# Kernel optimization log

Hardware: AMD Instinct MI355X
Metric: run time of the kernel (lower is better)

Reference implementation:

```python
import jax, jax.numpy as jnp
import numpy as np
import math

B, T, IN_DIM = 4, 1024, 64
D, H, L, DFF = 1024, 16, 4, 4096
N_STEPS = 24
MAXLEN = 2048
DK = D // H


def _pos_encoding(max_len, d):
    pos = np.arange(max_len, dtype=np.float32)[:, None]
    div = np.exp(np.arange(0, d, 2, dtype=np.float32) * (-math.log(10000.0) / d))
    pe = np.zeros((max_len, d), dtype=np.float32)
    pe[:, 0::2] = np.sin(pos * div)
    pe[:, 1::2] = np.cos(pos * div)
    return jnp.asarray(pe)

_PE = _pos_encoding(MAXLEN, D)


def _lin(x, W, b):
    # torch Linear convention: W is (out, in)
    return x @ W.T + b


def _mha(q, kv, Wq, bq, Wk, bk, Wv, bv, Wo, bo):
    Bq, Tq, _ = q.shape
    Tk = kv.shape[1]
    Qh = _lin(q, Wq, bq).reshape(Bq, Tq, H, DK).transpose(0, 2, 1, 3)
    Kh = _lin(kv, Wk, bk).reshape(Bq, Tk, H, DK).transpose(0, 2, 1, 3)
    Vh = _lin(kv, Wv, bv).reshape(Bq, Tk, H, DK).transpose(0, 2, 1, 3)
    scores = jnp.einsum('bhqd,bhkd->bhqk', Qh, Kh) / math.sqrt(DK)
    probs = jax.nn.softmax(scores, axis=-1)
    out = jnp.einsum('bhqk,bhkd->bhqd', probs, Vh)
    out = out.transpose(0, 2, 1, 3).reshape(Bq, Tq, D)
    return _lin(out, Wo, bo)


def _ffn(x, W1, b1, W2, b2):
    return _lin(jax.nn.relu(_lin(x, W1, b1)), W2, b2)


def _ln(x, g, b, eps=1e-5):
    mu = jnp.mean(x, axis=-1, keepdims=True)
    var = jnp.var(x, axis=-1, keepdims=True)
    return (x - mu) / jnp.sqrt(var + eps) * g + b


def setup_inputs() -> dict:
    key = jax.random.key(0)
    ks = iter(jax.random.split(key, 64))
    def w(shape, s=0.02):
        return jax.random.normal(next(ks), shape, jnp.float32) * s
    inp = {'x': jax.random.normal(next(ks), (B, T, IN_DIM), jnp.float32)}
    inp['in_W'] = w((D, IN_DIM)); inp['in_b'] = jnp.zeros((D,), jnp.float32)
    for p in ['enc', 'dec']:
        for n in ['Wq', 'Wk', 'Wv', 'Wo']:
            inp[f'{p}_{n}'] = w((L, D, D))
            inp[f'{p}_b{n[1].lower()}'] = jnp.zeros((L, D), jnp.float32)
    for p in ['ffe', 'ffd']:
        inp[f'{p}_W1'] = w((DFF, D)); inp[f'{p}_b1'] = jnp.zeros((DFF,), jnp.float32)
        inp[f'{p}_W2'] = w((D, DFF)); inp[f'{p}_b2'] = jnp.zeros((D,), jnp.float32)
    for p in ['ne', 'nd']:
        inp[f'{p}_g'] = jnp.ones((D,), jnp.float32); inp[f'{p}_b'] = jnp.zeros((D,), jnp.float32)
    inp['out_W'] = w((1, D)); inp['out_b'] = jnp.zeros((1,), jnp.float32)
    inp['temb_W'] = w((D, 1)); inp['temb_b'] = jnp.zeros((D,), jnp.float32)
    return inp


def reference(x, in_W, in_b,
              enc_Wq, enc_bq, enc_Wk, enc_bk, enc_Wv, enc_bv, enc_Wo, enc_bo,
              ffe_W1, ffe_b1, ffe_W2, ffe_b2, ne_g, ne_b,
              dec_Wq, dec_bq, dec_Wk, dec_bk, dec_Wv, dec_bv, dec_Wo, dec_bo,
              ffd_W1, ffd_b1, ffd_W2, ffd_b2, nd_g, nd_b,
              out_W, out_b, temb_W, temb_b):
    batch, seq, _ = x.shape
    h = _lin(x, in_W, in_b) + _PE[:seq]
    for l in range(L):
        h = _mha(h, h, enc_Wq[l], enc_bq[l], enc_Wk[l], enc_bk[l],
                 enc_Wv[l], enc_bv[l], enc_Wo[l], enc_bo[l])
        h = _ln(h + _ffn(h, ffe_W1, ffe_b1, ffe_W2, ffe_b2), ne_g, ne_b)
    dec = jnp.zeros((batch, 1, D), x.dtype)
    preds = []
    for _ in range(N_STEPS):
        d = dec + _PE[:dec.shape[1]]
        for l in range(L):
            # same layer weights used for self- and cross-attention, as in source
            d = _mha(d, d, dec_Wq[l], dec_bq[l], dec_Wk[l], dec_bk[l],
                     dec_Wv[l], dec_bv[l], dec_Wo[l], dec_bo[l])
            d = _mha(d, h, dec_Wq[l], dec_bq[l], dec_Wk[l], dec_bk[l],
                     dec_Wv[l], dec_bv[l], dec_Wo[l], dec_bo[l])
            d = _ln(d + _ffn(d, ffd_W1, ffd_b1, ffd_W2, ffd_b2), nd_g, nd_b)
        step = _lin(d[:, -1, :], out_W, out_b)        # (B, 1)
        preds.append(step[:, None, :])                 # (B, 1, 1)
        emb = _lin(step, temb_W, temb_b)[:, None, :]   # (B, 1, D)
        dec = jnp.concatenate([dec, emb], axis=1)
    return jnp.concatenate(preds, axis=1)              # (B, n_steps, 1)
```

## Files before the change

### kernel.cpp

```cpp
#include <hip/hip_runtime.h>
#include <math.h>

#define DM    1024
#define NH    16
#define DKH   64
#define NL    4
#define DFFN  4096
#define BB    4
#define TT    1024
#define NSTEP 24
#define BT    (BB*TT)
#define MD    (BB*NSTEP)
#define CSPLIT 8
#define CKEYS  (TT/CSPLIT)
#define PSTRIDE ((size_t)MD*DM)

typedef __attribute__((ext_vector_type(8))) short s16x8;
typedef __attribute__((ext_vector_type(4))) short s16x4;
typedef __attribute__((ext_vector_type(4))) float f32x4;

__device__ inline short f2b(float f){
  unsigned u = __float_as_uint(f);
  u += 0x7fffu + ((u>>16)&1u);
  return (short)(u>>16);
}
__device__ inline float b2f(short h){
  return __uint_as_float(((unsigned)(unsigned short)h)<<16);
}

__device__ inline float wave_sum(float v){
  #pragma unroll
  for (int off=1; off<64; off<<=1) v += __shfl_xor(v, off, 64);
  return v;
}

__global__ __launch_bounds__(256)
void split_kernel(const float* __restrict__ X, short* __restrict__ Hi,
                  short* __restrict__ Lo, int n8)
{
  const size_t i = (size_t)blockIdx.x*256 + threadIdx.x;
  if (i >= (size_t)n8) return;
  const float4 v0 = *(const float4*)(X + i*8);
  const float4 v1 = *(const float4*)(X + i*8 + 4);
  const float f[8] = {v0.x,v0.y,v0.z,v0.w,v1.x,v1.y,v1.z,v1.w};
  s16x8 hv, lv;
  #pragma unroll
  for (int e=0;e<8;e++){
    const short h = f2b(f[e]);
    hv[e] = h;
    lv[e] = f2b(f[e] - b2f(h));
  }
  *(s16x8*)(Hi + i*8) = hv;
  *(s16x8*)(Lo + i*8) = lv;
}

__global__ void zero_kernel(float* __restrict__ p, int n) {
  int i = blockIdx.x*256 + threadIdx.x;
  if (i < n) p[i] = 0.f;
}

__global__ __launch_bounds__(256)
void k_transpose(const float* __restrict__ A, float* __restrict__ At)
{
  __shared__ float tile[32][33];
  const int bx = blockIdx.x & 31, by = blockIdx.x >> 5;
  const int x0 = bx*32, y0 = by*32;
  const int tid = threadIdx.x;
  for (int i=tid; i<1024; i+=256){
    const int r = i>>5, c = i&31;
    tile[r][c] = A[(size_t)(y0+r)*DM + x0+c];
  }
  __syncthreads();
  for (int i=tid; i<1024; i+=256){
    const int r = i>>5, c = i&31;
    At[(size_t)(x0+r)*DM + y0+c] = tile[c][r];
  }
}

__global__ __launch_bounds__(256)
void k_bc(const float* __restrict__ Wq, const float* __restrict__ bo,
          const float* __restrict__ bq, float* __restrict__ bc)
{
  const int row = blockIdx.x, tid = threadIdx.x;
  float s = 0.f;
  for (int j=tid; j<DM; j+=256) s += Wq[(size_t)row*DM + j]*bo[j];
  s = wave_sum(s);
  __shared__ float r4[4];
  if ((tid&63)==0) r4[tid>>6] = s;
  __syncthreads();
  if (tid==0) bc[row] = r4[0]+r4[1]+r4[2]+r4[3] + bq[row];
}

__global__ __launch_bounds__(256)
void add_pe_split(const float* __restrict__ h, short* __restrict__ Hi,
                  short* __restrict__ Lo)
{
  const int row = blockIdx.x;
  const int pos = row & (TT-1);
  const int d = threadIdx.x*4;
  const float4 a = *(const float4*)(h + (size_t)row*DM + d);
  const float c1 = -9.210340371976184f / 1024.0f;
  const float e0 = expf((float)d * c1);
  const float e1 = expf((float)(d+2) * c1);
  const float a0 = (float)pos * e0, a1 = (float)pos * e1;
  const float v[4] = {a.x + sinf(a0), a.y + cosf(a0), a.z + sinf(a1), a.w + cosf(a1)};
  s16x4 hv, lv;
  #pragma unroll
  for (int e=0;e<4;e++){
    const short hb = f2b(v[e]);
    hv[e] = hb;
    lv[e] = f2b(v[e] - b2f(hb));
  }
  *(s16x4*)(Hi + (size_t)row*DM + d) = hv;
  *(s16x4*)(Lo + (size_t)row*DM + d) = lv;
}

template<int ACT, int OUT_MODE>
__global__ __launch_bounds__(256, 2)
void gemm_split(const short* __restrict__ Ahi, const short* __restrict__ Alo,
                const short* __restrict__ Bhi, const short* __restrict__ Blo,
                const float* __restrict__ bias,
                float* __restrict__ C, short* __restrict__ Chi, short* __restrict__ Clo,
                int M, int N, int K)
{
  __shared__ __align__(16) short lA[2][128][40];
  __shared__ __align__(16) short lB[2][128][40];
  const int tid = threadIdx.x;
  const int m0 = blockIdx.x*128, n0 = blockIdx.y*128;
  const int lane = tid & 63, w = tid >> 6;
  const int wr = w >> 1, wc = w & 1;
  const int fr = lane & 15, fq = lane >> 4;

  f32x4 acc[4][4];
  #pragma unroll
  for (int i=0;i<4;i++)
    #pragma unroll
    for (int j=0;j<4;j++) acc[i][j] = (f32x4){0.f,0.f,0.f,0.f};

  for (int k0 = 0; k0 < K; k0 += 32) {
    __syncthreads();
    #pragma unroll
    for (int j=0;j<2;j++){
      const int cc = tid + j*256;
      const int row = cc >> 2, kq = cc & 3;
      const size_t ga = (size_t)(m0+row)*K + k0 + kq*8;
      const size_t gb = (size_t)(n0+row)*K + k0 + kq*8;
      *(s16x8*)&lA[0][row][kq*8] = *(const s16x8*)(Ahi + ga);
      *(s16x8*)&lA[1][row][kq*8] = *(const s16x8*)(Alo + ga);
      *(s16x8*)&lB[0][row][kq*8] = *(const s16x8*)(Bhi + gb);
      *(s16x8*)&lB[1][row][kq*8] = *(const s16x8*)(Blo + gb);
    }
    __syncthreads();
    s16x8 ah[4], al[4], bh[4], bl[4];
    #pragma unroll
    for (int i=0;i<4;i++){
      ah[i] = *(const s16x8*)&lA[0][wr*64+i*16+fr][fq*8];
      al[i] = *(const s16x8*)&lA[1][wr*64+i*16+fr][fq*8];
    }
    #pragma unroll
    for (int j=0;j<4;j++){
      bh[j] = *(const s16x8*)&lB[0][wc*64+j*16+fr][fq*8];
      bl[j] = *(const s16x8*)&lB[1][wc*64+j*16+fr][fq*8];
    }
    #pragma unroll
    for (int i=0;i<4;i++)
      #pragma unroll
      for (int j=0;j<4;j++){
        acc[i][j] = __builtin_amdgcn_mfma_f32_16x16x32_bf16(ah[i], bh[j], acc[i][j], 0,0,0);
        acc[i][j] = __builtin_amdgcn_mfma_f32_16x16x32_bf16(ah[i], bl[j], acc[i][j], 0,0,0);
        acc[i][j] = __builtin_amdgcn_mfma_f32_16x16x32_bf16(al[i], bh[j], acc[i][j], 0,0,0);
      }
  }
  #pragma unroll
  for (int j=0;j<4;j++){
    const int col = n0 + wc*64 + j*16 + fr;
    const float bv = bias[col];
    #pragma unroll
    for (int i=0;i<4;i++){
      const int row0 = m0 + wr*64 + i*16 + fq*4;
      #pragma unroll
      for (int r=0;r<4;r++){
        float v = acc[i][j][r] + bv;
        if (ACT==1) v = fmaxf(v, 0.f);
        const size_t idx = (size_t)(row0+r)*N + col;
        if (OUT_MODE==0 || OUT_MODE==2) C[idx] = v;
        if (OUT_MODE==1 || OUT_MODE==2){
          const short hb = f2b(v);
          Chi[idx] = hb;
          Clo[idx] = f2b(v - b2f(hb));
        }
        if (OUT_MODE==3) Chi[idx] = f2b(v);
      }
    }
  }
}

__global__ __launch_bounds__(256)
void attn_enc(const float* __restrict__ Qg, const float* __restrict__ Kg,
              const float* __restrict__ Vg, short* __restrict__ Ohi,
              short* __restrict__ Olo)
{
  const int bh = blockIdx.y;
  const int b = bh >> 4, hh = bh & 15;
  const int row = blockIdx.x*256 + threadIdx.x;
  const size_t base = ((size_t)b*TT)*DM + hh*DKH;
  float q[64];
  {
    const float* qp = Qg + base + (size_t)row*DM;
    #pragma unroll
    for (int d4=0; d4<16; d4++){
      const float4 v = *(const float4*)(qp + d4*4);
      q[d4*4+0]=v.x; q[d4*4+1]=v.y; q[d4*4+2]=v.z; q[d4*4+3]=v.w;
    }
  }
  float o[64];
  #pragma unroll
  for (int d=0;d<64;d++) o[d]=0.f;
  float m = -INFINITY, l = 0.f;
  __shared__ float Ks[64][68];
  __shared__ float Vs[64][68];
  for (int kt=0; kt<TT; kt+=64) {
    __syncthreads();
    #pragma unroll
    for (int t=0;t<4;t++){
      const int fi = threadIdx.x + t*256;
      const int j = fi>>4, dq = fi&15;
      *(float4*)&Ks[j][dq*4] = *(const float4*)(Kg + base + (size_t)(kt+j)*DM + dq*4);
      *(float4*)&Vs[j][dq*4] = *(const float4*)(Vg + base + (size_t)(kt+j)*DM + dq*4);
    }
    __syncthreads();
    for (int j=0;j<64;j++){
      float s0=0.f,s1=0.f,s2=0.f,s3=0.f;
      #pragma unroll
      for (int d=0; d<64; d+=4){
        s0 = fmaf(q[d+0], Ks[j][d+0], s0);
        s1 = fmaf(q[d+1], Ks[j][d+1], s1);
        s2 = fmaf(q[d+2], Ks[j][d+2], s2);
        s3 = fmaf(q[d+3], Ks[j][d+3], s3);
      }
      const float s = ((s0+s1)+(s2+s3)) * 0.125f;
      if (s > m) {
        const float f = __expf(m - s);
        l *= f;
        #pragma unroll
        for (int d=0;d<64;d++) o[d] *= f;
        m = s;
      }
      const float p = __expf(s - m);
      l += p;
      #pragma unroll
      for (int d=0;d<64;d++) o[d] = fmaf(p, Vs[j][d], o[d]);
    }
  }
  const float inv = 1.f / l;
  #pragma unroll
  for (int d8=0; d8<8; d8++){
    s16x8 hv, lv;
    #pragma unroll
    for (int e=0;e<8;e++){
      const float f = o[d8*8+e]*inv;
      const short hb = f2b(f);
      hv[e] = hb;
      lv[e] = f2b(f - b2f(hb));
    }
    *(s16x8*)(Ohi + base + (size_t)row*DM + d8*8) = hv;
    *(s16x8*)(Olo + base + (size_t)row*DM + d8*8) = lv;
  }
}

__global__ __launch_bounds__(256)
void ln_add_split(const float* __restrict__ X, const float* __restrict__ Y,
                  const float* __restrict__ g, const float* __restrict__ be,
                  short* __restrict__ Ohi, short* __restrict__ Olo)
{
  const size_t row = blockIdx.x;
  const int tid = threadIdx.x;
  const float4 a = *(const float4*)(X + row*DM + tid*4);
  const float4 b = *(const float4*)(Y + row*DM + tid*4);
  const float v0=a.x+b.x, v1=a.y+b.y, v2=a.z+b.z, v3=a.w+b.w;
  float s = v0+v1+v2+v3;
  float q = v0*v0+v1*v1+v2*v2+v3*v3;
  s = wave_sum(s); q = wave_sum(q);
  __shared__ float rs[4], rq[4];
  if ((tid&63)==0){ rs[tid>>6]=s; rq[tid>>6]=q; }
  __syncthreads();
  const float S = rs[0]+rs[1]+rs[2]+rs[3];
  const float Q = rq[0]+rq[1]+rq[2]+rq[3];
  const float mean = S * (1.f/DM);
  const float var  = Q * (1.f/DM) - mean*mean;
  const float rstd = rsqrtf(var + 1e-5f);
  const float4 gv = *(const float4*)(g  + tid*4);
  const float4 bv = *(const float4*)(be + tid*4);
  const float v[4] = {(v0-mean)*rstd*gv.x + bv.x, (v1-mean)*rstd*gv.y + bv.y,
                      (v2-mean)*rstd*gv.z + bv.z, (v3-mean)*rstd*gv.w + bv.w};
  s16x4 hv, lv;
  #pragma unroll
  for (int e=0;e<4;e++){
    const short hb = f2b(v[e]);
    hv[e] = hb;
    lv[e] = f2b(v[e] - b2f(hb));
  }
  *(s16x4*)(Ohi + row*DM + tid*4) = hv;
  *(s16x4*)(Olo + row*DM + tid*4) = lv;
}


template<int MR>
__global__ __launch_bounds__(256)
void gemm_dec(const short* __restrict__ Ahi, const short* __restrict__ Alo,
              const short* __restrict__ B0hi, const short* __restrict__ B0lo,
              const short* __restrict__ B1hi, const short* __restrict__ B1lo,
              const short* __restrict__ B2hi, const short* __restrict__ B2lo,
              float* __restrict__ part, int N, int K, int KS)
{
  const short* Bhi = (blockIdx.z==0) ? B0hi : (blockIdx.z==1 ? B1hi : B2hi);
  const short* Blo = (blockIdx.z==0) ? B0lo : (blockIdx.z==1 ? B1lo : B2lo);
  float* P = part + ((size_t)blockIdx.z*KS + blockIdx.y)*(size_t)MD*N;
  const int KK = K / KS;
  const int kbase = blockIdx.y * KK;
  const int n0 = blockIdx.x * 128;
  __shared__ __align__(16) short lA[2][96][40];
  __shared__ __align__(16) short lB[2][128][40];
  const int tid = threadIdx.x;
  const int lane = tid & 63, w = tid >> 6;
  const int fr = lane & 15, fq = lane >> 4;
  constexpr int CH = MR*128;

  f32x4 acc[MR][2];
  #pragma unroll
  for (int i=0;i<MR;i++){ acc[i][0]=(f32x4){0,0,0,0}; acc[i][1]=(f32x4){0,0,0,0}; }

  for (int k0 = kbase; k0 < kbase + KK; k0 += 32) {
    __syncthreads();
    #pragma unroll
    for (int t=0; t<(CH+255)/256; t++){
      const int cc = tid + t*256;
      if (cc < CH){
        const int row = cc>>3, hl = (cc>>2)&1, kq = cc&3;
        const short* src = hl ? Alo : Ahi;
        *(s16x8*)&lA[hl][row][kq*8] = *(const s16x8*)(src + (size_t)row*K + k0 + kq*8);
      }
    }
    #pragma unroll
    for (int t=0; t<4; t++){
      const int cc = tid + t*256;
      const int row = cc>>3, hl = (cc>>2)&1, kq = cc&3;
      const short* src = hl ? Blo : Bhi;
      *(s16x8*)&lB[hl][row][kq*8] = *(const s16x8*)(src + (size_t)(n0+row)*K + k0 + kq*8);
    }
    __syncthreads();
    s16x8 bh[2], bl[2];
    #pragma unroll
    for (int j=0;j<2;j++){
      bh[j] = *(const s16x8*)&lB[0][w*32+j*16+fr][fq*8];
      bl[j] = *(const s16x8*)&lB[1][w*32+j*16+fr][fq*8];
    }
    #pragma unroll
    for (int i=0;i<MR;i++){
      const s16x8 ah = *(const s16x8*)&lA[0][i*16+fr][fq*8];
      const s16x8 al = *(const s16x8*)&lA[1][i*16+fr][fq*8];
      #pragma unroll
      for (int j=0;j<2;j++){
        acc[i][j] = __builtin_amdgcn_mfma_f32_16x16x32_bf16(ah, bh[j], acc[i][j], 0,0,0);
        acc[i][j] = __builtin_amdgcn_mfma_f32_16x16x32_bf16(ah, bl[j], acc[i][j], 0,0,0);
        acc[i][j] = __builtin_amdgcn_mfma_f32_16x16x32_bf16(al, bh[j], acc[i][j], 0,0,0);
      }
    }
  }
  #pragma unroll
  for (int j=0;j<2;j++){
    const int col = n0 + w*32 + j*16 + fr;
    #pragma unroll
    for (int i=0;i<MR;i++){
      const int row0 = i*16 + fq*4;
      #pragma unroll
      for (int r=0;r<4;r++)
        P[(size_t)(row0+r)*N + col] = acc[i][j][r];
    }
  }
}

template<int ACT, int MODE>
__global__ __launch_bounds__(256)
void reduce_dec(const float* __restrict__ part,
                const float* __restrict__ b0, const float* __restrict__ b1,
                const float* __restrict__ b2,
                float* __restrict__ o0, float* __restrict__ o1, float* __restrict__ o2,
                short* __restrict__ ohi, short* __restrict__ olo,
                int N, int KS)
{
  const int idx = blockIdx.x*256 + threadIdx.x;
  const int z = blockIdx.y;
  const float* P = part + (size_t)z*KS*(size_t)MD*N;
  const float* bias = (z==0)?b0:(z==1?b1:b2);
  float* out = (z==0)?o0:(z==1?o1:o2);
  float s = 0.f;
  for (int ks=0; ks<KS; ks++) s += P[(size_t)ks*MD*N + idx];
  s += bias[idx & (N-1)];
  if (ACT==1) s = fmaxf(s, 0.f);
  if (MODE==0 || MODE==2) out[idx] = s;
  if (MODE==1 || MODE==2){
    if (z==0){
      const short hb = f2b(s);
      ohi[idx] = hb;
      olo[idx] = f2b(s - b2f(hb));
    }
  }
}

__global__ __launch_bounds__(256)
void attn_qkv(const float* __restrict__ part,
              const float* __restrict__ lbq, const float* __restrict__ lbk,
              const float* __restrict__ lbv,
              short* __restrict__ Ohi, short* __restrict__ Olo, int n)
{
  const int bh = blockIdx.x, b = bh >> 4, hh = bh & 15;
  const size_t obase = (size_t)b*DM + hh*DKH;
  __shared__ float Qs[NSTEP][68], Ks[NSTEP][68], Vs[NSTEP][68];
  __shared__ float P[NSTEP][28];
  const int tid = threadIdx.x;
  for (int t = tid; t < 3*n*16; t += 256){
    const int tensor = t / (n*16);
    const int fi = t - tensor*(n*16);
    const int row = fi >> 4, q4 = fi & 15;
    const int col0 = hh*DKH + q4*4;
    const float* bias = (tensor==0?lbq:(tensor==1?lbk:lbv));
    float4 a;
    a.x = bias[col0]; a.y = bias[col0+1]; a.z = bias[col0+2]; a.w = bias[col0+3];
    const size_t eoff = (size_t)(row*4+b)*DM + col0;
    #pragma unroll
    for (int ks=0; ks<8; ks++){
      const float4 p = *(const float4*)(part + (size_t)(tensor*8+ks)*PSTRIDE + eoff);
      a.x+=p.x; a.y+=p.y; a.z+=p.z; a.w+=p.w;
    }
    float (*dst)[68] = (tensor==0?Qs:(tensor==1?Ks:Vs));
    *(float4*)&dst[row][q4*4] = a;
  }
  __syncthreads();
  for (int idx = tid; idx < n*n; idx += 256){
    const int i = idx / n, j = idx - i*n;
    float s0=0.f,s1=0.f,s2=0.f,s3=0.f;
    #pragma unroll
    for (int d=0; d<64; d+=4){
      s0 = fmaf(Qs[i][d+0], Ks[j][d+0], s0);
      s1 = fmaf(Qs[i][d+1], Ks[j][d+1], s1);
      s2 = fmaf(Qs[i][d+2], Ks[j][d+2], s2);
      s3 = fmaf(Qs[i][d+3], Ks[j][d+3], s3);
    }
    P[i][j] = ((s0+s1)+(s2+s3))*0.125f;
  }
  __syncthreads();
  if (tid < n){
    float mm = -INFINITY;
    for (int j=0;j<n;j++) mm = fmaxf(mm, P[tid][j]);
    float l = 0.f;
    for (int j=0;j<n;j++){ const float p = __expf(P[tid][j]-mm); P[tid][j]=p; l+=p; }
    const float inv = 1.f/l;
    for (int j=0;j<n;j++) P[tid][j] *= inv;
  }
  __syncthreads();
  for (int idx = tid; idx < n*64; idx += 256){
    const int i = idx >> 6, d = idx & 63;
    float s = 0.f;
    for (int j=0;j<n;j++) s = fmaf(P[i][j], Vs[j][d], s);
    const short hb = f2b(s);
    const size_t o = obase + (size_t)(i*4)*DM + d;
    Ohi[o] = hb;
    Olo[o] = f2b(s - b2f(hb));
  }
}

__global__ __launch_bounds__(256)
void attn_cross_part(const float* __restrict__ Qg, const short* __restrict__ Kc,
                     const short* __restrict__ Vc, float* __restrict__ opart,
                     float* __restrict__ mlpart, int n)
{
  const int ks = blockIdx.x, bh = blockIdx.y;
  const int b = bh >> 4, hh = bh & 15;
  __shared__ float Qs[NSTEP][68];
  __shared__ short KVs[CKEYS][72];
  __shared__ float S[NSTEP][132];
  const int tid = threadIdx.x;
  const size_t qbase = (size_t)b*DM + hh*DKH;
  for (int t=tid; t<n*16; t+=256){
    const int row = t>>4, q4 = t&15;
    *(float4*)&Qs[row][q4*4] = *(const float4*)(Qg + qbase + (size_t)(row*4)*DM + q4*4);
  }
  const size_t kbase = ((size_t)b*TT + (size_t)ks*CKEYS)*DM + hh*DKH;
  for (int t=tid; t<CKEYS*8; t+=256){
    const int row = t>>3, d8 = t&7;
    *(s16x8*)&KVs[row][d8*8] = *(const s16x8*)(Kc + kbase + (size_t)row*DM + d8*8);
  }
  __syncthreads();
  for (int idx=tid; idx<n*128; idx+=256){
    const int i = idx >> 7, j = idx & 127;
    float s0=0.f,s1=0.f,s2=0.f,s3=0.f;
    #pragma unroll
    for (int d=0; d<64; d+=4){
      s0 = fmaf(Qs[i][d+0], b2f(KVs[j][d+0]), s0);
      s1 = fmaf(Qs[i][d+1], b2f(KVs[j][d+1]), s1);
      s2 = fmaf(Qs[i][d+2], b2f(KVs[j][d+2]), s2);
      s3 = fmaf(Qs[i][d+3], b2f(KVs[j][d+3]), s3);
    }
    S[i][j] = ((s0+s1)+(s2+s3))*0.125f;
  }
  __syncthreads();
  for (int t=tid; t<CKEYS*8; t+=256){
    const int row = t>>3, d8 = t&7;
    *(s16x8*)&KVs[row][d8*8] = *(const s16x8*)(Vc + kbase + (size_t)row*DM + d8*8);
  }
  if (tid < n){
    float mm=-INFINITY;
    for (int j=0;j<CKEYS;j++) mm = fmaxf(mm, S[tid][j]);
    float l=0.f;
    for (int j=0;j<CKEYS;j++){ const float p=__expf(S[tid][j]-mm); S[tid][j]=p; l+=p; }
    mlpart[((size_t)bh*CSPLIT+ks)*(2*NSTEP) + tid*2+0] = mm;
    mlpart[((size_t)bh*CSPLIT+ks)*(2*NSTEP) + tid*2+1] = l;
  }
  __syncthreads();
  for (int idx=tid; idx<n*64; idx+=256){
    const int i = idx >> 6, d = idx & 63;
    float s=0.f;
    for (int j=0;j<CKEYS;j++) s = fmaf(S[i][j], b2f(KVs[j][d]), s);
    opart[(((size_t)bh*CSPLIT+ks)*NSTEP + i)*DKH + d] = s;
  }
}

__global__ __launch_bounds__(256)
void attn_cross_comb(const float* __restrict__ opart, const float* __restrict__ mlpart,
                     short* __restrict__ Ohi, short* __restrict__ Olo, int n)
{
  const int bh = blockIdx.x;
  const int idx = blockIdx.y*256 + threadIdx.x;
  const int i = idx >> 6, d = idx & 63;
  if (i >= n) return;
  float M = -INFINITY;
  #pragma unroll
  for (int s=0;s<CSPLIT;s++)
    M = fmaxf(M, mlpart[((size_t)bh*CSPLIT+s)*(2*NSTEP) + i*2]);
  float acc = 0.f, L = 0.f;
  #pragma unroll
  for (int s=0;s<CSPLIT;s++){
    const float mm = mlpart[((size_t)bh*CSPLIT+s)*(2*NSTEP) + i*2+0];
    const float ll = mlpart[((size_t)bh*CSPLIT+s)*(2*NSTEP) + i*2+1];
    const float f = __expf(mm - M);
    acc = fmaf(f, opart[(((size_t)bh*CSPLIT+s)*NSTEP + i)*DKH + d], acc);
    L   = fmaf(f, ll, L);
  }
  const int b = bh >> 4, hh = bh & 15;
  const float v = acc / L;
  const short hb = f2b(v);
  const size_t o = ((size_t)(i*4+b))*DM + hh*DKH + d;
  Ohi[o] = hb;
  Olo[o] = f2b(v - b2f(hb));
}

__global__ __launch_bounds__(256)
void k_lnr(const float* __restrict__ part, const float* __restrict__ bias,
           const float* __restrict__ X, const float* __restrict__ g,
           const float* __restrict__ be,
           float* __restrict__ Outf, short* __restrict__ Ohi, short* __restrict__ Olo)
{
  const int row = blockIdx.x;
  __shared__ float rs[4], rq[4];
  const int tid = threadIdx.x;
  float a0=0.f,a1=0.f,a2=0.f,a3=0.f;
  #pragma unroll
  for (int ks=0; ks<16; ks++){
    const float4 p = *(const float4*)(part + (size_t)ks*PSTRIDE + (size_t)row*DM + tid*4);
    a0+=p.x; a1+=p.y; a2+=p.z; a3+=p.w;
  }
  const float4 bvv = *(const float4*)(bias + tid*4);
  const float4 xv  = *(const float4*)(X + (size_t)row*DM + tid*4);
  const float v0=a0+bvv.x+xv.x, v1=a1+bvv.y+xv.y, v2=a2+bvv.z+xv.z, v3=a3+bvv.w+xv.w;
  float s = v0+v1+v2+v3;
  float q = v0*v0+v1*v1+v2*v2+v3*v3;
  s = wave_sum(s); q = wave_sum(q);
  if ((tid&63)==0){ rs[tid>>6]=s; rq[tid>>6]=q; }
  __syncthreads();
  const float S = rs[0]+rs[1]+rs[2]+rs[3];
  const float Q = rq[0]+rq[1]+rq[2]+rq[3];
  const float mean = S * (1.f/DM);
  const float var  = Q * (1.f/DM) - mean*mean;
  const float rstd = rsqrtf(var + 1e-5f);
  const float4 gv = *(const float4*)(g  + tid*4);
  const float4 bv2 = *(const float4*)(be + tid*4);
  const float v[4] = {(v0-mean)*rstd*gv.x + bv2.x, (v1-mean)*rstd*gv.y + bv2.y,
                      (v2-mean)*rstd*gv.z + bv2.z, (v3-mean)*rstd*gv.w + bv2.w};
  float4 of; of.x=v[0]; of.y=v[1]; of.z=v[2]; of.w=v[3];
  *(float4*)(Outf + (size_t)row*DM + tid*4) = of;
  s16x4 hv, lv;
  #pragma unroll
  for (int e=0;e<4;e++){
    const short hb = f2b(v[e]);
    hv[e] = hb;
    lv[e] = f2b(v[e] - b2f(hb));
  }
  *(s16x4*)(Ohi + (size_t)row*DM + tid*4) = hv;
  *(s16x4*)(Olo + (size_t)row*DM + tid*4) = lv;
}

__global__ __launch_bounds__(256)
void k_out(const float* __restrict__ Dv, const float* __restrict__ outW,
           const float* __restrict__ outB, const float* __restrict__ tembW,
           const float* __restrict__ tembB, float* __restrict__ dout,
           short* __restrict__ Dphi, short* __restrict__ Dplo, int s)
{
  const int b = blockIdx.x;
  __shared__ float red[4];
  __shared__ float stepv;
  const int tid = threadIdx.x;
  const float* drow = Dv + ((size_t)(s*4 + b))*DM;
  const float4 dv4 = *(const float4*)(drow + tid*4);
  const float4 wv = *(const float4*)(outW + tid*4);
  float p = dv4.x*wv.x + dv4.y*wv.y + dv4.z*wv.z + dv4.w*wv.w;
  p = wave_sum(p);
  if ((tid&63)==0) red[tid>>6] = p;
  __syncthreads();
  if (tid==0){
    const float sv = red[0]+red[1]+red[2]+red[3] + outB[0];
    stepv = sv;
    dout[b*NSTEP + s] = sv;
  }
  __syncthreads();
  const float sv = stepv;
  if (s+1 < NSTEP){
    const int d = tid*4, pos = s+1;
    const float4 tw = *(const float4*)(tembW + d);
    const float4 tb = *(const float4*)(tembB + d);
    const float c1 = -9.210340371976184f / 1024.0f;
    const float e0 = expf((float)d * c1);
    const float e1 = expf((float)(d+2) * c1);
    const float a0 = (float)pos * e0, a1 = (float)pos * e1;
    const float v[4] = { fmaf(sv, tw.x, tb.x) + sinf(a0),
                         fmaf(sv, tw.y, tb.y) + cosf(a0),
                         fmaf(sv, tw.z, tb.z) + sinf(a1),
                         fmaf(sv, tw.w, tb.w) + cosf(a1) };
    s16x4 hv, lv;
    #pragma unroll
    for (int e=0;e<4;e++){
      const short hb = f2b(v[e]);
      hv[e] = hb;
      lv[e] = f2b(v[e] - b2f(hb));
    }
    const size_t o = (size_t)(pos*4 + b)*DM + d;
    *(s16x4*)(Dphi + o) = hv;
    *(s16x4*)(Dplo + o) = lv;
  }
}

__global__ __launch_bounds__(256)
void k_init0(short* __restrict__ Dphi, short* __restrict__ Dplo)
{
  const int b = blockIdx.x;
  const int d = threadIdx.x*4;
  const float v[4] = {0.f, 1.f, 0.f, 1.f};
  s16x4 hv, lv;
  #pragma unroll
  for (int e=0;e<4;e++){
    const short hb = f2b(v[e]);
    hv[e] = hb;
    lv[e] = f2b(v[e] - b2f(hb));
  }
  *(s16x4*)(Dphi + (size_t)b*DM + d) = hv;
  *(s16x4*)(Dplo + (size_t)b*DM + d) = lv;
}

extern "C" void kernel_launch(void* const* d_in, const int* in_sizes, int n_in,
                              void* d_out, int out_size, void* d_ws, size_t ws_size,
                              hipStream_t stream)
{
  (void)in_sizes; (void)n_in; (void)out_size; (void)ws_size;
  const float* x      = (const float*)d_in[0];
  const float* in_W   = (const float*)d_in[1];
  const float* in_b   = (const float*)d_in[2];
  const float* enc_Wq = (const float*)d_in[3];
  const float* enc_bq = (const float*)d_in[4];
  const float* enc_Wk = (const float*)d_in[5];
  const float* enc_bk = (const float*)d_in[6];
  const float* enc_Wv = (const float*)d_in[7];
  const float* enc_bv = (const float*)d_in[8];
  const float* enc_Wo = (const float*)d_in[9];
  const float* enc_bo = (const float*)d_in[10];
  const float* dec_Wq = (const float*)d_in[11];
  const float* dec_bq = (const float*)d_in[12];
  const float* dec_Wk = (const float*)d_in[13];
  const float* dec_bk = (const float*)d_in[14];
  const float* dec_Wv = (const float*)d_in[15];
  const float* dec_bv = (const float*)d_in[16];
  const float* dec_Wo = (const float*)d_in[17];
  const float* dec_bo = (const float*)d_in[18];
  const float* ffe_W1 = (const float*)d_in[19];
  const float* ffe_b1 = (const float*)d_in[20];
  const float* ffe_W2 = (const float*)d_in[21];
  const float* ffe_b2 = (const float*)d_in[22];
  const float* ffd_W1 = (const float*)d_in[23];
  const float* ffd_b1 = (const float*)d_in[24];
  const float* ffd_W2 = (const float*)d_in[25];
  const float* ffd_b2 = (const float*)d_in[26];
  const float* ne_g   = (const float*)d_in[27];
  const float* ne_b   = (const float*)d_in[28];
  const float* nd_g   = (const float*)d_in[29];
  const float* nd_b   = (const float*)d_in[30];
  const float* out_W  = (const float*)d_in[31];
  const float* out_b  = (const float*)d_in[32];
  const float* temb_W = (const float*)d_in[33];
  const float* temb_b = (const float*)d_in[34];
  float* dout = (float*)d_out;

  float* ws = (float*)d_ws;
  size_t off = 0;
  auto alloc  = [&](size_t n){ n = (n+3)&~(size_t)3; float* p = ws + off; off += n; return p; };
  auto allocS = [&](size_t n){ size_t nf = ((n+1)/2 + 3)&~(size_t)3; short* p = (short*)(ws + off); off += nf; return p; };

  short* hshi = allocS((size_t)BT*DM);
  short* hslo = allocS((size_t)BT*DM);
  float* h    = alloc((size_t)BT*DM);
  float* hn   = h;
  float* t0   = alloc((size_t)BT*DM);
  float* t1   = alloc((size_t)BT*DM);
  float* t2   = alloc((size_t)BT*DM);
  short* t3hi = allocS((size_t)BT*DM);
  short* t3lo = allocS((size_t)BT*DM);
  short* hnhi = allocS((size_t)BT*DM);
  short* hnlo = allocS((size_t)BT*DM);
  float* t4   = alloc((size_t)BT*DM);
  float* part = t4;
  short* fmhi = (short*)t0;
  short* fmlo = fmhi + (size_t)BT*DFFN;
  short* kcb  = allocS((size_t)NL*BT*DM);
  short* vcb  = allocS((size_t)NL*BT*DM);
  short* xshi = allocS((size_t)BT*64);
  short* xslo = allocS((size_t)BT*64);
  short* iwhi = allocS((size_t)DM*64);
  short* iwlo = allocS((size_t)DM*64);
  short* w0hi = allocS((size_t)DM*DM); short* w0lo = allocS((size_t)DM*DM);
  short* w1hi = allocS((size_t)DM*DM); short* w1lo = allocS((size_t)DM*DM);
  short* w2hi = allocS((size_t)DM*DM); short* w2lo = allocS((size_t)DM*DM);
  short* w3hi = allocS((size_t)DM*DM); short* w3lo = allocS((size_t)DM*DM);
  short* wfhi = allocS((size_t)DFFN*DM); short* wflo = allocS((size_t)DFFN*DM);
  short* wf2hi= allocS((size_t)DM*DFFN); short* wf2lo= allocS((size_t)DM*DFFN);
  float* bqo  = alloc((size_t)NL*DM);
  float* zbuf = alloc((size_t)DM);
  float* dq   = alloc((size_t)MD*DM);
  float* dbuf = alloc((size_t)MD*DM);
  short* dphi = allocS((size_t)MD*DM);  short* dplo = allocS((size_t)MD*DM);
  short* dlhi = allocS((size_t)MD*DM);  short* dllo = allocS((size_t)MD*DM);
  short* dxhi = allocS((size_t)MD*DM);  short* dxlo = allocS((size_t)MD*DM);
  short* dahi = allocS((size_t)MD*DM);  short* dalo = allocS((size_t)MD*DM);
  short* dmhi = allocS((size_t)MD*DFFN);short* dmlo = allocS((size_t)MD*DFFN);
  float* opart= alloc((size_t)BB*NH*CSPLIT*NSTEP*DKH);
  float* mlp  = alloc((size_t)BB*NH*CSPLIT*2*NSTEP);

  const size_t MM = (size_t)DM*DM;
  short* dwq = (short*)t0;
  short* dwk = (short*)t1;
  short* dwv = (short*)t2;
  short* dwo = (short*)h;
  short* fw1h = t3hi; short* fw1l = t3lo;
  short* fw2h = hnhi; short* fw2l = hnlo;
  short* wch  = hshi; short* wcl  = hslo;
  float* wotf = t4;
  float* wcf  = t4 + MM;

  auto cvt = [&](const float* src, short* hi, short* lo, size_t n){
    split_kernel<<<(int)((n/8 + 255)/256), 256, 0, stream>>>(src, hi, lo, (int)(n/8));
  };

  cvt(x,    xshi, xslo, (size_t)BT*64);
  cvt(in_W, iwhi, iwlo, (size_t)DM*64);
  cvt(ffe_W1, wfhi,  wflo,  (size_t)DFFN*DM);
  cvt(ffe_W2, wf2hi, wf2lo, (size_t)DM*DFFN);
  zero_kernel<<<(DM+255)/256, 256, 0, stream>>>(zbuf, DM);

  gemm_split<0,0><<<dim3(BT/128, DM/128), 256, 0, stream>>>(
      xshi, xslo, iwhi, iwlo, in_b, h, (short*)nullptr, (short*)nullptr, BT, DM, 64);
  add_pe_split<<<BT, 256, 0, stream>>>(h, hshi, hslo);

  for (int l=0; l<NL; ++l) {
    const size_t wo = (size_t)l*DM*DM, bo_ = (size_t)l*DM;
    cvt(enc_Wq+wo, w0hi, w0lo, MM);
    cvt(enc_Wk+wo, w1hi, w1lo, MM);
    cvt(enc_Wv+wo, w2hi, w2lo, MM);
    cvt(enc_Wo+wo, w3hi, w3lo, MM);
    gemm_split<0,0><<<dim3(32,8),256,0,stream>>>(hshi, hslo, w0hi, w0lo, enc_bq+bo_,
        t0, (short*)nullptr, (short*)nullptr, BT, DM, DM);
    gemm_split<0,0><<<dim3(32,8),256,0,stream>>>(hshi, hslo, w1hi, w1lo, enc_bk+bo_,
        t1, (short*)nullptr, (short*)nullptr, BT, DM, DM);
    gemm_split<0,0><<<dim3(32,8),256,0,stream>>>(hshi, hslo, w2hi, w2lo, enc_bv+bo_,
        t2, (short*)nullptr, (short*)nullptr, BT, DM, DM);
    attn_enc<<<dim3(TT/256, BB*NH),256,0,stream>>>(t0, t1, t2, t3hi, t3lo);
    gemm_split<0,2><<<dim3(32,8),256,0,stream>>>(t3hi, t3lo, w3hi, w3lo, enc_bo+bo_,
        hn, hnhi, hnlo, BT, DM, DM);
    gemm_split<1,1><<<dim3(32,32),256,0,stream>>>(hnhi, hnlo, wfhi, wflo, ffe_b1,
        (float*)nullptr, fmhi, fmlo, BT, DFFN, DM);
    gemm_split<0,0><<<dim3(32,8),256,0,stream>>>(fmhi, fmlo, wf2hi, wf2lo, ffe_b2,
        t4, (short*)nullptr, (short*)nullptr, BT, DM, DFFN);
    ln_add_split<<<BT,256,0,stream>>>(hn, t4, ne_g, ne_b, hshi, hslo);
  }

  for (int l=0; l<NL; ++l) {
    const size_t wo = (size_t)l*DM*DM, bo_ = (size_t)l*DM;
    cvt(dec_Wk+wo, w0hi, w0lo, MM);
    cvt(dec_Wv+wo, w1hi, w1lo, MM);
    gemm_split<0,3><<<dim3(32,8),256,0,stream>>>(hshi, hslo, w0hi, w0lo, dec_bk+bo_,
        (float*)nullptr, kcb+(size_t)l*BT*DM, (short*)nullptr, BT, DM, DM);
    gemm_split<0,3><<<dim3(32,8),256,0,stream>>>(hshi, hslo, w1hi, w1lo, dec_bv+bo_,
        (float*)nullptr, vcb+(size_t)l*BT*DM, (short*)nullptr, BT, DM, DM);
  }

  for (int l=0; l<NL; ++l) {
    const size_t wo = (size_t)l*DM*DM;
    cvt(dec_Wq+wo, dwq + (size_t)l*2*MM, dwq + (size_t)l*2*MM + MM, MM);
    cvt(dec_Wk+wo, dwk + (size_t)l*2*MM, dwk + (size_t)l*2*MM + MM, MM);
    cvt(dec_Wv+wo, dwv + (size_t)l*2*MM, dwv + (size_t)l*2*MM + MM, MM);
    cvt(dec_Wo+wo, dwo + (size_t)l*2*MM, dwo + (size_t)l*2*MM + MM, MM);
  }
  cvt(ffd_W1, fw1h, fw1l, (size_t)DFFN*DM);
  cvt(ffd_W2, fw2h, fw2l, (size_t)DM*DFFN);
  for (int l=0; l<NL; ++l) {
    const size_t wo = (size_t)l*DM*DM, bo_ = (size_t)l*DM;
    k_transpose<<<1024, 256, 0, stream>>>(dec_Wo+wo, wotf);
    cvt(wotf,      w0hi, w0lo, MM);
    cvt(dec_Wq+wo, w1hi, w1lo, MM);
    gemm_split<0,0><<<dim3(8,8),256,0,stream>>>(w1hi, w1lo, w0hi, w0lo, zbuf,
        wcf, (short*)nullptr, (short*)nullptr, DM, DM, DM);
    k_bc<<<DM, 256, 0, stream>>>(dec_Wq+wo, dec_bo+bo_, dec_bq+bo_, bqo+bo_);
    cvt(wcf, wch + (size_t)l*MM, wcl + (size_t)l*MM, MM);
  }

  #define GD(MRv, grid, ...) do { switch(MRv){ \
    case 1: gemm_dec<1><<<grid,256,0,stream>>>(__VA_ARGS__); break; \
    case 2: gemm_dec<2><<<grid,256,0,stream>>>(__VA_ARGS__); break; \
    case 3: gemm_dec<3><<<grid,256,0,stream>>>(__VA_ARGS__); break; \
    case 4: gemm_dec<4><<<grid,256,0,stream>>>(__VA_ARGS__); break; \
    case 5: gemm_dec<5><<<grid,256,0,stream>>>(__VA_ARGS__); break; \
    default: gemm_dec<6><<<grid,256,0,stream>>>(__VA_ARGS__); break; } } while(0)

  k_init0<<<BB, 256, 0, stream>>>(dphi, dplo);
  for (int s=0; s<NSTEP; ++s){
    const int n = s+1, rows = 4*n;
    const int Mt = (rows + 15) & ~15;
    const int MR = Mt >> 4;
    for (int l=0; l<NL; ++l){
      const short* qh = dwq + (size_t)l*2*MM; const short* ql = qh + MM;
      const short* kh = dwk + (size_t)l*2*MM; const short* kl = kh + MM;
      const short* vh = dwv + (size_t)l*2*MM; const short* vl = vh + MM;
      const short* oh = dwo + (size_t)l*2*MM; const short* ol = oh + MM;
      const short* ch = wch + (size_t)l*MM;   const short* cl = wcl + (size_t)l*MM;
      const float* lbq = dec_bq + (size_t)l*DM;
      const float* lbk = dec_bk + (size_t)l*DM;
      const float* lbv = dec_bv + (size_t)l*DM;
      const float* lbo = dec_bo + (size_t)l*DM;
      const float* lbc = bqo + (size_t)l*DM;
      const short* in_hi = (l==0) ? dphi : dlhi;
      const short* in_lo = (l==0) ? dplo : dllo;
      GD(MR, dim3(8,8,3), in_hi,in_lo, qh,ql, kh,kl, vh,vl, part, DM, DM, 8);
      attn_qkv<<<BB*NH,256,0,stream>>>(part, lbq, lbk, lbv, dahi, dalo, n);
      GD(MR, dim3(8,8,1), dahi,dalo, ch,cl, ch,cl, ch,cl, part, DM, DM, 8);
      reduce_dec<0,0><<<dim3(Mt*4,1),256,0,stream>>>(part, lbc, lbc, lbc,
          dq, dq, dq, (short*)nullptr, (short*)nullptr, DM, 8);
      attn_cross_part<<<dim3(CSPLIT, BB*NH),256,0,stream>>>(dq,
          kcb + (size_t)l*BT*DM, vcb + (size_t)l*BT*DM, opart, mlp, n);
      attn_cross_comb<<<dim3(BB*NH, 6),256,0,stream>>>(opart, mlp, dahi, dalo, n);
      GD(MR, dim3(8,8,1), dahi,dalo, oh,ol, oh,ol, oh,ol, part, DM, DM, 8);
      reduce_dec<0,2><<<dim3(Mt*4,1),256,0,stream>>>(part, lbo, lbo, lbo,
          dbuf, dbuf, dbuf, dxhi, dxlo, DM, 8);
      GD(MR, dim3(32,8,1), dxhi,dxlo, fw1h,fw1l, fw1h,fw1l, fw1h,fw1l, part, DFFN, DM, 8);
      reduce_dec<1,1><<<dim3(Mt*16,1),256,0,stream>>>(part, ffd_b1, ffd_b1, ffd_b1,
          (float*)nullptr,(float*)nullptr,(float*)nullptr, dmhi, dmlo, DFFN, 8);
      GD(MR, dim3(8,16,1), dmhi,dmlo, fw2h,fw2l, fw2h,fw2l, fw2h,fw2l, part, DM, DFFN, 16);
      k_lnr<<<rows,256,0,stream>>>(part, ffd_b2, dbuf, nd_g, nd_b, dbuf, dlhi, dllo);
    }
    k_out<<<BB, 256, 0, stream>>>(dbuf, out_W, out_b, temb_W, temb_b, dout,
        dphi, dplo, s);
  }
  #undef GD
}
```

Before: 13.60 ms.

## Fuse split-K partial reductions into consumer GEMM prologues and LayerNorm

Removes the separate reduce_dec kernels in the decoder loop. The split-K partial sums, plus bias and ReLU, are now summed and converted to hi/lo bf16 while loading the A tile inside a new gemm_dec_r kernel, inside attn_cross_part's Q load, and inside k_lnr. This cuts three kernel launches per layer-step and the intermediate write/read round trips, at the cost of every N-tile block redundantly re-reading and re-summing the 8 partial A slices.

Measured after the change: 13.22 ms. -2.8%, faster.

```diff
diff --git a/kernel.cpp b/kernel.cpp
--- a/kernel.cpp
+++ b/kernel.cpp
@@ -14,6 +14,7 @@
 #define CSPLIT 8
 #define CKEYS  (TT/CSPLIT)
 #define PSTRIDE ((size_t)MD*DM)
+#define PSTRIDE_F ((size_t)MD*DFFN)
 
 typedef __attribute__((ext_vector_type(8))) short s16x8;
 typedef __attribute__((ext_vector_type(4))) short s16x4;
@@ -380,30 +381,94 @@
   }
 }
 
-template<int ACT, int MODE>
-__global__ __launch_bounds__(256)
-void reduce_dec(const float* __restrict__ part,
-                const float* __restrict__ b0, const float* __restrict__ b1,
-                const float* __restrict__ b2,
-                float* __restrict__ o0, float* __restrict__ o1, float* __restrict__ o2,
-                short* __restrict__ ohi, short* __restrict__ olo,
-                int N, int KS)
-{
-  const int idx = blockIdx.x*256 + threadIdx.x;
-  const int z = blockIdx.y;
-  const float* P = part + (size_t)z*KS*(size_t)MD*N;
-  const float* bias = (z==0)?b0:(z==1?b1:b2);
-  float* out = (z==0)?o0:(z==1?o1:o2);
-  float s = 0.f;
-  for (int ks=0; ks<KS; ks++) s += P[(size_t)ks*MD*N + idx];
-  s += bias[idx & (N-1)];
-  if (ACT==1) s = fmaxf(s, 0.f);
-  if (MODE==0 || MODE==2) out[idx] = s;
-  if (MODE==1 || MODE==2){
-    if (z==0){
-      const short hb = f2b(s);
-      ohi[idx] = hb;
-      olo[idx] = f2b(s - b2f(hb));
+template<int MR, int AACT>
+__global__ __launch_bounds__(256)
+void gemm_dec_r(const float* __restrict__ PA, const float* __restrict__ biasA,
+                const short* __restrict__ Bhi, const short* __restrict__ Blo,
+                float* __restrict__ part, int N, int K, int KS)
+{
+  float* P = part + (size_t)blockIdx.y*(size_t)MD*N;
+  const int KK = K / KS;
+  const int kbase = blockIdx.y * KK;
+  const int n0 = blockIdx.x * 128;
+  __shared__ __align__(16) short lA[2][96][40];
+  __shared__ __align__(16) short lB[2][128][40];
+  const int tid = threadIdx.x;
+  const int lane = tid & 63, w = tid >> 6;
+  const int fr = lane & 15, fq = lane >> 4;
+  constexpr int CH = MR*128;
+  const size_t psA = (size_t)MD*K;
+
+  f32x4 acc[MR][2];
+  #pragma unroll
+  for (int i=0;i<MR;i++){ acc[i][0]=(f32x4){0,0,0,0}; acc[i][1]=(f32x4){0,0,0,0}; }
+
+  for (int k0 = kbase; k0 < kbase + KK; k0 += 32) {
+    __syncthreads();
+    #pragma unroll
+    for (int t=0; t<(CH+255)/256; t++){
+      const int cc = tid + t*256;
+      if (cc < CH){
+        const int row = cc>>3, q = cc&7;
+        const int k = k0 + q*4;
+        float4 a = *(const float4*)(biasA + k);
+        const float* src = PA + (size_t)row*K + k;
+        #pragma unroll
+        for (int p=0;p<8;p++){
+          const float4 v = *(const float4*)(src + (size_t)p*psA);
+          a.x+=v.x; a.y+=v.y; a.z+=v.z; a.w+=v.w;
+        }
+        if (AACT){
+          a.x=fmaxf(a.x,0.f); a.y=fmaxf(a.y,0.f);
+          a.z=fmaxf(a.z,0.f); a.w=fmaxf(a.w,0.f);
+        }
+        const float vv[4] = {a.x,a.y,a.z,a.w};
+        s16x4 hv, lv;
+        #pragma unroll
+        for (int e=0;e<4;e++){
+          const short hb = f2b(vv[e]);
+          hv[e] = hb;
+          lv[e] = f2b(vv[e] - b2f(hb));
+        }
+        *(s16x4*)&lA[0][row][q*4] = hv;
+        *(s16x4*)&lA[1][row][q*4] = lv;
+      }
+    }
+    #pragma unroll
+    for (int t=0; t<4; t++){
+      const int cc = tid + t*256;
+      const int row = cc>>3, hl = (cc>>2)&1, kq = cc&3;
+      const short* src = hl ? Blo : Bhi;
+      *(s16x8*)&lB[hl][row][kq*8] = *(const s16x8*)(src + (size_t)(n0+row)*K + k0 + kq*8);
+    }
+    __syncthreads();
+    s16x8 bh[2], bl[2];
+    #pragma unroll
+    for (int j=0;j<2;j++){
+      bh[j] = *(const s16x8*)&lB[0][w*32+j*16+fr][fq*8];
+      bl[j] = *(const s16x8*)&lB[1][w*32+j*16+fr][fq*8];
+    }
+    #pragma unroll
+    for (int i=0;i<MR;i++){
+      const s16x8 ah = *(const s16x8*)&lA[0][i*16+fr][fq*8];
+      const s16x8 al = *(const s16x8*)&lA[1][i*16+fr][fq*8];
+      #pragma unroll
+      for (int j=0;j<2;j++){
+        acc[i][j] = __builtin_amdgcn_mfma_f32_16x16x32_bf16(ah, bh[j], acc[i][j], 0,0,0);
+        acc[i][j] = __builtin_amdgcn_mfma_f32_16x16x32_bf16(ah, bl[j], acc[i][j], 0,0,0);
+        acc[i][j] = __builtin_amdgcn_mfma_f32_16x16x32_bf16(al, bh[j], acc[i][j], 0,0,0);
+      }
+    }
+  }
+  #pragma unroll
+  for (int j=0;j<2;j++){
+    const int col = n0 + w*32 + j*16 + fr;
+    #pragma unroll
+    for (int i=0;i<MR;i++){
+      const int row0 = i*16 + fq*4;
+      #pragma unroll
+      for (int r=0;r<4;r++)
+        P[(size_t)(row0+r)*N + col] = acc[i][j][r];
     }
   }
 }
@@ -471,9 +536,9 @@
 }
 
 __global__ __launch_bounds__(256)
-void attn_cross_part(const float* __restrict__ Qg, const short* __restrict__ Kc,
-                     const short* __restrict__ Vc, float* __restrict__ opart,
-                     float* __restrict__ mlpart, int n)
+void attn_cross_part(const float* __restrict__ Qpart, const float* __restrict__ lbc,
+                     const short* __restrict__ Kc, const short* __restrict__ Vc,
+                     float* __restrict__ opart, float* __restrict__ mlpart, int n)
 {
   const int ks = blockIdx.x, bh = blockIdx.y;
   const int b = bh >> 4, hh = bh & 15;
@@ -481,10 +546,18 @@
   __shared__ short KVs[CKEYS][72];
   __shared__ float S[NSTEP][132];
   const int tid = threadIdx.x;
-  const size_t qbase = (size_t)b*DM + hh*DKH;
   for (int t=tid; t<n*16; t+=256){
     const int row = t>>4, q4 = t&15;
-    *(float4*)&Qs[row][q4*4] = *(const float4*)(Qg + qbase + (size_t)(row*4)*DM + q4*4);
+    const int col0 = hh*DKH + q4*4;
+    float4 a;
+    a.x = lbc[col0]; a.y = lbc[col0+1]; a.z = lbc[col0+2]; a.w = lbc[col0+3];
+    const size_t eoff = (size_t)(row*4+b)*DM + col0;
+    #pragma unroll
+    for (int p=0; p<8; p++){
+      const float4 v = *(const float4*)(Qpart + (size_t)p*PSTRIDE + eoff);
+      a.x+=v.x; a.y+=v.y; a.z+=v.z; a.w+=v.w;
+    }
+    *(float4*)&Qs[row][q4*4] = a;
   }
   const size_t kbase = ((size_t)b*TT + (size_t)ks*CKEYS)*DM + hh*DKH;
   for (int t=tid; t<CKEYS*8; t+=256){
@@ -556,23 +629,35 @@
 }
 
 __global__ __launch_bounds__(256)
-void k_lnr(const float* __restrict__ part, const float* __restrict__ bias,
-           const float* __restrict__ X, const float* __restrict__ g,
-           const float* __restrict__ be,
+void k_lnr(const float* __restrict__ partF, const float* __restrict__ fb2,
+           const float* __restrict__ partR, const float* __restrict__ lbo,
+           const float* __restrict__ g, const float* __restrict__ be,
            float* __restrict__ Outf, short* __restrict__ Ohi, short* __restrict__ Olo)
 {
   const int row = blockIdx.x;
   __shared__ float rs[4], rq[4];
   const int tid = threadIdx.x;
-  float a0=0.f,a1=0.f,a2=0.f,a3=0.f;
+  float a0,a1,a2,a3;
+  {
+    const float4 bv = *(const float4*)(fb2 + tid*4);
+    a0=bv.x; a1=bv.y; a2=bv.z; a3=bv.w;
+  }
   #pragma unroll
   for (int ks=0; ks<16; ks++){
-    const float4 p = *(const float4*)(part + (size_t)ks*PSTRIDE + (size_t)row*DM + tid*4);
+    const float4 p = *(const float4*)(partF + (size_t)ks*PSTRIDE + (size_t)row*DM + tid*4);
     a0+=p.x; a1+=p.y; a2+=p.z; a3+=p.w;
   }
-  const float4 bvv = *(const float4*)(bias + tid*4);
-  const float4 xv  = *(const float4*)(X + (size_t)row*DM + tid*4);
-  const float v0=a0+bvv.x+xv.x, v1=a1+bvv.y+xv.y, v2=a2+bvv.z+xv.z, v3=a3+bvv.w+xv.w;
+  float r0,r1,r2,r3;
+  {
+    const float4 bv = *(const float4*)(lbo + tid*4);
+    r0=bv.x; r1=bv.y; r2=bv.z; r3=bv.w;
+  }
+  #pragma unroll
+  for (int ks=0; ks<8; ks++){
+    const float4 p = *(const float4*)(partR + (size_t)ks*PSTRIDE + (size_t)row*DM + tid*4);
+    r0+=p.x; r1+=p.y; r2+=p.z; r3+=p.w;
+  }
+  const float v0=a0+r0, v1=a1+r1, v2=a2+r2, v3=a3+r3;
   float s = v0+v1+v2+v3;
   float q = v0*v0+v1*v1+v2*v2+v3*v3;
   s = wave_sum(s); q = wave_sum(q);
@@ -725,7 +810,7 @@
   short* hnhi = allocS((size_t)BT*DM);
   short* hnlo = allocS((size_t)BT*DM);
   float* t4   = alloc((size_t)BT*DM);
-  float* part = t4;
+  float* partA = t4;
   short* fmhi = (short*)t0;
   short* fmlo = fmhi + (size_t)BT*DFFN;
   short* kcb  = allocS((size_t)NL*BT*DM);
@@ -742,13 +827,12 @@
   short* wf2hi= allocS((size_t)DM*DFFN); short* wf2lo= allocS((size_t)DM*DFFN);
   float* bqo  = alloc((size_t)NL*DM);
   float* zbuf = alloc((size_t)DM);
-  float* dq   = alloc((size_t)MD*DM);
   float* dbuf = alloc((size_t)MD*DM);
   short* dphi = allocS((size_t)MD*DM);  short* dplo = allocS((size_t)MD*DM);
   short* dlhi = allocS((size_t)MD*DM);  short* dllo = allocS((size_t)MD*DM);
-  short* dxhi = allocS((size_t)MD*DM);  short* dxlo = allocS((size_t)MD*DM);
   short* dahi = allocS((size_t)MD*DM);  short* dalo = allocS((size_t)MD*DM);
-  short* dmhi = allocS((size_t)MD*DFFN);short* dmlo = allocS((size_t)MD*DFFN);
+  float* partB = alloc((size_t)16*MD*DM);
+  float* partC = alloc((size_t)8*MD*DM);
   float* opart= alloc((size_t)BB*NH*CSPLIT*NSTEP*DKH);
   float* mlp  = alloc((size_t)BB*NH*CSPLIT*2*NSTEP);
 
@@ -836,6 +920,13 @@
     case 4: gemm_dec<4><<<grid,256,0,stream>>>(__VA_ARGS__); break; \
     case 5: gemm_dec<5><<<grid,256,0,stream>>>(__VA_ARGS__); break; \
     default: gemm_dec<6><<<grid,256,0,stream>>>(__VA_ARGS__); break; } } while(0)
+  #define GDR(MRv, AACT, grid, ...) do { switch(MRv){ \
+    case 1: gemm_dec_r<1,AACT><<<grid,256,0,stream>>>(__VA_ARGS__); break; \
+    case 2: gemm_dec_r<2,AACT><<<grid,256,0,stream>>>(__VA_ARGS__); break; \
+    case 3: gemm_dec_r<3,AACT><<<grid,256,0,stream>>>(__VA_ARGS__); break; \
+    case 4: gemm_dec_r<4,AACT><<<grid,256,0,stream>>>(__VA_ARGS__); break; \
+    case 5: gemm_dec_r<5,AACT><<<grid,256,0,stream>>>(__VA_ARGS__); break; \
+    default: gemm_dec_r<6,AACT><<<grid,256,0,stream>>>(__VA_ARGS__); break; } } while(0)
 
   k_init0<<<BB, 256, 0, stream>>>(dphi, dplo);
   for (int s=0; s<NSTEP; ++s){
@@ -855,25 +946,21 @@
       const float* lbc = bqo + (size_t)l*DM;
       const short* in_hi = (l==0) ? dphi : dlhi;
       const short* in_lo = (l==0) ? dplo : dllo;
-      GD(MR, dim3(8,8,3), in_hi,in_lo, qh,ql, kh,kl, vh,vl, part, DM, DM, 8);
-      attn_qkv<<<BB*NH,256,0,stream>>>(part, lbq, lbk, lbv, dahi, dalo, n);
-      GD(MR, dim3(8,8,1), dahi,dalo, ch,cl, ch,cl, ch,cl, part, DM, DM, 8);
-      reduce_dec<0,0><<<dim3(Mt*4,1),256,0,stream>>>(part, lbc, lbc, lbc,
-          dq, dq, dq, (short*)nullptr, (short*)nullptr, DM, 8);
-      attn_cross_part<<<dim3(CSPLIT, BB*NH),256,0,stream>>>(dq,
+      GD(MR, dim3(8,8,3), in_hi,in_lo, qh,ql, kh,kl, vh,vl, partA, DM, DM, 8);
+      attn_qkv<<<BB*NH,256,0,stream>>>(partA, lbq, lbk, lbv, dahi, dalo, n);
+      GD(MR, dim3(8,8,1), dahi,dalo, ch,cl, ch,cl, ch,cl, partB, DM, DM, 8);
+      attn_cross_part<<<dim3(CSPLIT, BB*NH),256,0,stream>>>(partB, lbc,
           kcb + (size_t)l*BT*DM, vcb + (size_t)l*BT*DM, opart, mlp, n);
       attn_cross_comb<<<dim3(BB*NH, 6),256,0,stream>>>(opart, mlp, dahi, dalo, n);
-      GD(MR, dim3(8,8,1), dahi,dalo, oh,ol, oh,ol, oh,ol, part, DM, DM, 8);
-      reduce_dec<0,2><<<dim3(Mt*4,1),256,0,stream>>>(part, lbo, lbo, lbo,
-          dbuf, dbuf, dbuf, dxhi, dxlo, DM, 8);
-      GD(MR, dim3(32,8,1), dxhi,dxlo, fw1h,fw1l, fw1h,fw1l, fw1h,fw1l, part, DFFN, DM, 8);
-      reduce_dec<1,1><<<dim3(Mt*16,1),256,0,stream>>>(part, ffd_b1, ffd_b1, ffd_b1,
-          (float*)nullptr,(float*)nullptr,(float*)nullptr, dmhi, dmlo, DFFN, 8);
-      GD(MR, dim3(8,16,1), dmhi,dmlo, fw2h,fw2l, fw2h,fw2l, fw2h,fw2l, part, DM, DFFN, 16);
-      k_lnr<<<rows,256,0,stream>>>(part, ffd_b2, dbuf, nd_g, nd_b, dbuf, dlhi, dllo);
+      GD(MR, dim3(8,8,1), dahi,dalo, oh,ol, oh,ol, oh,ol, partC, DM, DM, 8);
+      GDR(MR, 0, dim3(32,8), partC, lbo, fw1h, fw1l, partA, DFFN, DM, 8);
+      GDR(MR, 1, dim3(8,16), partA, ffd_b1, fw2h, fw2l, partB, DM, DFFN, 16);
+      k_lnr<<<rows,256,0,stream>>>(partB, ffd_b2, partC, lbo, nd_g, nd_b,
+          dbuf, dlhi, dllo);
     }
     k_out<<<BB, 256, 0, stream>>>(dbuf, out_W, out_b, temb_W, temb_b, dout,
         dphi, dplo, s);
   }
   #undef GD
-}
+  #undef GDR
+}
```
